# Optimization experiments

Hardware: AMD Instinct MI355X
Metric: run time of the kernel (lower is better)

Reference implementation:

```python
import jax, jax.numpy as jnp
import numpy as np


def setup_inputs() -> dict:
    key = jax.random.key(0)
    k1, k2 = jax.random.split(key)
    N, C, V, D = 200000, 10, 2, 256
    y = jax.random.randint(k1, (N, C), 0, 2, dtype=jnp.int32)
    train_views = jax.random.normal(k2, (V, N, D), dtype=jnp.float32)
    return {"y": y, "train_views": train_views}


def reference(y, train_views):
    # Original torch code: for each view, for each class i, zero out rows where
    # y[:, i] == 1 (keep only where mask == 0), sum over nodes -> [D], and
    # concatenate across classes -> [C*D]. This is a masked per-class sum:
    #   out[v, i, d] = sum_n (y[n, i] == 0) * x[v, n, d]
    keep = (y == 0).astype(train_views.dtype)          # [N, C]
    out = jnp.einsum('nc,vnd->vcd', keep, train_views) # [V, C, D]
    V, C, D = out.shape
    return out.reshape(V, C * D)                       # concat of per-class sums
```

## Files before the change

kernel.cpp:

```cpp
#include <hip/hip_runtime.h>
#include <cstdint>

#define CCLS 10
#define DDIM 256
#define NCHUNK 256
#define UNR 8

typedef float f32x4 __attribute__((ext_vector_type(4)));

__device__ inline f32x4 ntload4(const f32x4* p) {
    return __builtin_nontemporal_load(p);
}
__device__ inline uint32_t rfl(uint32_t x) {
    return (uint32_t)__builtin_amdgcn_readfirstlane((int)x);
}

__global__ void pack_mask_kernel(const int* __restrict__ y, uint32_t* __restrict__ km, int N) {
    __shared__ int sy[256 * CCLS];
    const int base = blockIdx.x * 256;
    const int total = N * CCLS;
    for (int i = threadIdx.x; i < 256 * CCLS; i += 256) {
        int idx = base * CCLS + i;
        sy[i] = (idx < total) ? y[idx] : 1;
    }
    __syncthreads();
    const int n = base + threadIdx.x;
    if (n < N) {
        uint32_t m = 0;
        #pragma unroll
        for (int c = 0; c < CCLS; ++c)
            m |= (sy[threadIdx.x * CCLS + c] == 0 ? 1u : 0u) << c;
        km[n] = m;
    }
}

template <int EPI>
__global__ __launch_bounds__(256, 4) void masked_sum_kernel(
    const float* __restrict__ x,
    const uint32_t* __restrict__ km,
    const int* __restrict__ y,
    float* __restrict__ dst,
    int N, int rows_per_chunk, int nchunk)
{
    const int v = blockIdx.y;
    const int chunk = blockIdx.x;
    const int n0 = chunk * rows_per_chunk;
    const int n1 = min(n0 + rows_per_chunk, N);
    const int row = threadIdx.x >> 6;
    const int d4  = threadIdx.x & 63;

    f32x4 acc[CCLS];
    #pragma unroll
    for (int c = 0; c < CCLS; ++c) acc[c] = (f32x4){0.f, 0.f, 0.f, 0.f};

    const f32x4* __restrict__ xb =
        reinterpret_cast<const f32x4*>(x + (size_t)v * N * DDIM);

    auto inline_mask = [&](int n) -> uint32_t {
        uint32_t m = 0;
        #pragma unroll
        for (int c = 0; c < CCLS; ++c)
            m |= (y[n * CCLS + c] == 0 ? 1u : 0u) << c;
        return m;
    };

    int n = n0 + row;
    for (; n + 4 * (UNR - 1) < n1; n += 4 * UNR) {
        f32x4 xv[UNR];
        uint32_t mm[UNR];
        #pragma unroll
        for (int u = 0; u < UNR; ++u)
            xv[u] = ntload4(xb + (size_t)(n + 4 * u) * (DDIM / 4) + d4);
        #pragma unroll
        for (int u = 0; u < UNR; ++u)
            mm[u] = (EPI == 0) ? km[n + 4 * u] : inline_mask(n + 4 * u);
        #pragma unroll
        for (int u = 0; u < UNR; ++u) {
            const uint32_t m = rfl(mm[u]);
            #pragma unroll
            for (int c = 0; c < CCLS; ++c)
                acc[c] += (((m >> c) & 1u) ? 1.0f : 0.0f) * xv[u];
        }
    }
    for (; n < n1; n += 4) {
        f32x4 x0 = ntload4(xb + (size_t)n * (DDIM / 4) + d4);
        const uint32_t m = rfl((EPI == 0) ? km[n] : inline_mask(n));
        #pragma unroll
        for (int c = 0; c < CCLS; ++c)
            acc[c] += (((m >> c) & 1u) ? 1.0f : 0.0f) * x0;
    }

    __shared__ f32x4 lred[4][CCLS][DDIM / 4];
    #pragma unroll
    for (int c = 0; c < CCLS; ++c)
        lred[row][c][d4] = acc[c];
    __syncthreads();

    const f32x4* __restrict__ lf = &lred[0][0][0];
    if (EPI == 0) {
        f32x4* __restrict__ dstv = reinterpret_cast<f32x4*>(
            dst + ((size_t)v * nchunk + chunk) * (CCLS * DDIM));
        for (int j = threadIdx.x; j < CCLS * DDIM / 4; j += 256) {
            f32x4 s = (lf[j] + lf[640 + j]) + (lf[1280 + j] + lf[1920 + j]);
            dstv[j] = s;
        }
    } else {
        float* __restrict__ outv = dst + (size_t)v * (CCLS * DDIM);
        for (int j = threadIdx.x; j < CCLS * DDIM / 4; j += 256) {
            f32x4 s = (lf[j] + lf[640 + j]) + (lf[1280 + j] + lf[1920 + j]);
            atomicAdd(&outv[4 * j + 0], s.x);
            atomicAdd(&outv[4 * j + 1], s.y);
            atomicAdd(&outv[4 * j + 2], s.z);
            atomicAdd(&outv[4 * j + 3], s.w);
        }
    }
}

__global__ __launch_bounds__(256) void reduce_parts_kernel(
    const float* __restrict__ part, float* __restrict__ out, int nchunk)
{
    const int v = blockIdx.y;
    const int w = threadIdx.x >> 6, l = threadIdx.x & 63;
    const int colbase = blockIdx.x * 4;
    const int col = colbase + (l & 3);
    const int slot = l >> 2;
    const int cpw = nchunk / 4;
    const f32x4* __restrict__ b =
        reinterpret_cast<const f32x4*>(part) + (size_t)v * nchunk * (CCLS * DDIM / 4);

    f32x4 s = (f32x4){0.f, 0.f, 0.f, 0.f};
    #pragma unroll 4
    for (int ch = w * cpw + slot; ch < (w + 1) * cpw; ch += 16)
        s += b[(size_t)ch * (CCLS * DDIM / 4) + col];

    #pragma unroll
    for (int off = 4; off < 64; off <<= 1) {
        s.x += __shfl_xor(s.x, off);
        s.y += __shfl_xor(s.y, off);
        s.z += __shfl_xor(s.z, off);
        s.w += __shfl_xor(s.w, off);
    }

    __shared__ f32x4 lred[4][4];
    if (l < 4) lred[w][l] = s;
    __syncthreads();
    if (threadIdx.x < 4) {
        f32x4 t = (lred[0][threadIdx.x] + lred[1][threadIdx.x]) +
                  (lred[2][threadIdx.x] + lred[3][threadIdx.x]);
        reinterpret_cast<f32x4*>(out)[(size_t)v * (CCLS * DDIM / 4) + colbase + threadIdx.x] = t;
    }
}

extern "C" void kernel_launch(void* const* d_in, const int* in_sizes, int n_in,
                              void* d_out, int out_size, void* d_ws, size_t ws_size,
                              hipStream_t stream) {
    const int*   y = (const int*)d_in[0];
    const float* x = (const float*)d_in[1];
    float* out = (float*)d_out;

    const int N = in_sizes[0] / CCLS;
    const int V = in_sizes[1] / (N * DDIM);

    const size_t km_bytes   = ((size_t)N * sizeof(uint32_t) + 255) & ~(size_t)255;
    const size_t part_bytes = (size_t)V * NCHUNK * CCLS * DDIM * sizeof(float);

    const int rpc = (N + NCHUNK - 1) / NCHUNK;
    dim3 grid(NCHUNK, V);

    if (ws_size >= km_bytes + part_bytes) {
        uint32_t* km = (uint32_t*)d_ws;
        float* part = (float*)((char*)d_ws + km_bytes);
        pack_mask_kernel<<<(N + 255) / 256, 256, 0, stream>>>(y, km, N);
        masked_sum_kernel<0><<<grid, 256, 0, stream>>>(x, km, y, part, N, rpc, NCHUNK);
        reduce_parts_kernel<<<dim3(CCLS * DDIM / 4 / 4, V), 256, 0, stream>>>(part, out, NCHUNK);
    } else {
        hipMemsetAsync(d_out, 0, (size_t)out_size * sizeof(float), stream);
        masked_sum_kernel<2><<<grid, 256, 0, stream>>>(x, nullptr, y, out, N, rpc, NCHUNK);
    }
}
```

Before: 78.05 us.

## Fuse mask packing into sum kernel via LDS and software-pipeline row loads

Drops the separate pack_mask kernel. Each block now builds its chunk's class bitmasks straight from y into shared memory, while its first batch of x rows is already loading. The main loop is software-pipelined: it issues the next UNR row loads before accumulating the current ones. Launch bounds relax from 4 to 2 blocks per CU to make room for the extra registers. This removes one launch and the km round trip through global memory, at the cost of more registers and possibly lower occupancy.

```diff
diff --git a/kernel.cpp b/kernel.cpp
--- a/kernel.cpp
+++ b/kernel.cpp
@@ -5,6 +5,7 @@
 #define DDIM 256
 #define NCHUNK 256
 #define UNR 8
+#define RPC_MAX 800
 
 typedef float f32x4 __attribute__((ext_vector_type(4)));
 
@@ -15,29 +16,9 @@
     return (uint32_t)__builtin_amdgcn_readfirstlane((int)x);
 }
 
-__global__ void pack_mask_kernel(const int* __restrict__ y, uint32_t* __restrict__ km, int N) {
-    __shared__ int sy[256 * CCLS];
-    const int base = blockIdx.x * 256;
-    const int total = N * CCLS;
-    for (int i = threadIdx.x; i < 256 * CCLS; i += 256) {
-        int idx = base * CCLS + i;
-        sy[i] = (idx < total) ? y[idx] : 1;
-    }
-    __syncthreads();
-    const int n = base + threadIdx.x;
-    if (n < N) {
-        uint32_t m = 0;
-        #pragma unroll
-        for (int c = 0; c < CCLS; ++c)
-            m |= (sy[threadIdx.x * CCLS + c] == 0 ? 1u : 0u) << c;
-        km[n] = m;
-    }
-}
-
 template <int EPI>
-__global__ __launch_bounds__(256, 4) void masked_sum_kernel(
+__global__ __launch_bounds__(256, 2) void masked_sum_kernel(
     const float* __restrict__ x,
-    const uint32_t* __restrict__ km,
     const int* __restrict__ y,
     float* __restrict__ dst,
     int N, int rows_per_chunk, int nchunk)
@@ -46,51 +27,67 @@
     const int chunk = blockIdx.x;
     const int n0 = chunk * rows_per_chunk;
     const int n1 = min(n0 + rows_per_chunk, N);
+    const int nr = n1 - n0;
     const int row = threadIdx.x >> 6;
     const int d4  = threadIdx.x & 63;
+
+    __shared__ uint32_t smask[RPC_MAX];
+    __shared__ f32x4 lred[4][CCLS][DDIM / 4];
+
+    const f32x4* __restrict__ xb =
+        reinterpret_cast<const f32x4*>(x + (size_t)v * N * DDIM);
 
     f32x4 acc[CCLS];
     #pragma unroll
     for (int c = 0; c < CCLS; ++c) acc[c] = (f32x4){0.f, 0.f, 0.f, 0.f};
 
-    const f32x4* __restrict__ xb =
-        reinterpret_cast<const f32x4*>(x + (size_t)v * N * DDIM);
+    int n = n0 + row;
+    bool have = (n + 4 * (UNR - 1) < n1);
+    f32x4 xv[UNR];
+    if (have) {
+        #pragma unroll
+        for (int u = 0; u < UNR; ++u)
+            xv[u] = ntload4(xb + (size_t)(n + 4 * u) * (DDIM / 4) + d4);
+    }
 
-    auto inline_mask = [&](int n) -> uint32_t {
+    for (int r = threadIdx.x; r < nr; r += 256) {
+        const int* __restrict__ yr = y + (size_t)(n0 + r) * CCLS;
         uint32_t m = 0;
         #pragma unroll
         for (int c = 0; c < CCLS; ++c)
-            m |= (y[n * CCLS + c] == 0 ? 1u : 0u) << c;
-        return m;
-    };
+            m |= (yr[c] == 0 ? 1u : 0u) << c;
+        smask[r] = m;
+    }
+    __syncthreads();
 
-    int n = n0 + row;
-    for (; n + 4 * (UNR - 1) < n1; n += 4 * UNR) {
-        f32x4 xv[UNR];
-        uint32_t mm[UNR];
-        #pragma unroll
-        for (int u = 0; u < UNR; ++u)
-            xv[u] = ntload4(xb + (size_t)(n + 4 * u) * (DDIM / 4) + d4);
-        #pragma unroll
-        for (int u = 0; u < UNR; ++u)
-            mm[u] = (EPI == 0) ? km[n + 4 * u] : inline_mask(n + 4 * u);
+    while (have) {
+        const int nn = n + 4 * UNR;
+        const bool hnext = (nn + 4 * (UNR - 1) < n1);
+        f32x4 xn[UNR];
+        if (hnext) {
+            #pragma unroll
+            for (int u = 0; u < UNR; ++u)
+                xn[u] = ntload4(xb + (size_t)(nn + 4 * u) * (DDIM / 4) + d4);
+        }
         #pragma unroll
         for (int u = 0; u < UNR; ++u) {
-            const uint32_t m = rfl(mm[u]);
+            const uint32_t m = rfl(smask[n - n0 + 4 * u]);
             #pragma unroll
             for (int c = 0; c < CCLS; ++c)
                 acc[c] += (((m >> c) & 1u) ? 1.0f : 0.0f) * xv[u];
         }
+        #pragma unroll
+        for (int u = 0; u < UNR; ++u) xv[u] = xn[u];
+        n = nn; have = hnext;
     }
     for (; n < n1; n += 4) {
         f32x4 x0 = ntload4(xb + (size_t)n * (DDIM / 4) + d4);
-        const uint32_t m = rfl((EPI == 0) ? km[n] : inline_mask(n));
+        const uint32_t m = rfl(smask[n - n0]);
         #pragma unroll
         for (int c = 0; c < CCLS; ++c)
             acc[c] += (((m >> c) & 1u) ? 1.0f : 0.0f) * x0;
     }
 
-    __shared__ f32x4 lred[4][CCLS][DDIM / 4];
     #pragma unroll
     for (int c = 0; c < CCLS; ++c)
         lred[row][c][d4] = acc[c];
@@ -161,20 +158,19 @@
     const int N = in_sizes[0] / CCLS;
     const int V = in_sizes[1] / (N * DDIM);
 
-    const size_t km_bytes   = ((size_t)N * sizeof(uint32_t) + 255) & ~(size_t)255;
-    const size_t part_bytes = (size_t)V * NCHUNK * CCLS * DDIM * sizeof(float);
+    int nchunk = NCHUNK;
+    while ((N + nchunk - 1) / nchunk > RPC_MAX) nchunk += 64;
+    const int rpc = (N + nchunk - 1) / nchunk;
 
-    const int rpc = (N + NCHUNK - 1) / NCHUNK;
-    dim3 grid(NCHUNK, V);
+    const size_t part_bytes = (size_t)V * nchunk * CCLS * DDIM * sizeof(float);
+    dim3 grid(nchunk, V);
 
-    if (ws_size >= km_bytes + part_bytes) {
-        uint32_t* km = (uint32_t*)d_ws;
-        float* part = (float*)((char*)d_ws + km_bytes);
-        pack_mask_kernel<<<(N + 255) / 256, 256, 0, stream>>>(y, km, N);
-        masked_sum_kernel<0><<<grid, 256, 0, stream>>>(x, km, y, part, N, rpc, NCHUNK);
-        reduce_parts_kernel<<<dim3(CCLS * DDIM / 4 / 4, V), 256, 0, stream>>>(part, out, NCHUNK);
+    if (ws_size >= part_bytes) {
+        float* part = (float*)d_ws;
+        masked_sum_kernel<0><<<grid, 256, 0, stream>>>(x, y, part, N, rpc, nchunk);
+        reduce_parts_kernel<<<dim3(CCLS * DDIM / 16, V), 256, 0, stream>>>(part, out, nchunk);
     } else {
         hipMemsetAsync(d_out, 0, (size_t)out_size * sizeof(float), stream);
-        masked_sum_kernel<2><<<grid, 256, 0, stream>>>(x, nullptr, y, out, N, rpc, NCHUNK);
+        masked_sum_kernel<1><<<grid, 256, 0, stream>>>(x, y, out, N, rpc, nchunk);
     }
 }
```

Result: faster. 74.93 us (-4.0%).
